# Kernel tuning notes

Measured on AMD Instinct MI355X. Metric: run time of the kernel, lower is better.

Reference implementation:

```python
import jax, jax.numpy as jnp
import numpy as np

N, C, V, L = 32, 32, 400, 64
GH_IN, GH = 64, [128, 64]
NUM_GRAPHS, ORDER, K, ALPHA = 2, 2, 20, 0.05
OUT_CH = 32
CAT_CH = C * (NUM_GRAPHS * ORDER + 1)
BN_EPS = 1e-5


def setup_inputs() -> dict:
    key = jax.random.key(0)
    ks = jax.random.split(key, 12)
    s = lambda fan_in: 1.0 / np.sqrt(fan_in)
    return {
        "inputs": jax.random.normal(ks[0], (N, C, V, L), jnp.float32),
        "adj_mats": jax.random.normal(ks[1], (V, V, GH_IN), jnp.float32),
        # edge MLP: Linear(64->128), ReLU, Linear(128->64), ReLU, Linear(64->num_graphs)
        "mlp_w0": jax.random.normal(ks[2], (GH_IN, GH[0]), jnp.float32) * s(GH_IN),
        "mlp_b0": jnp.zeros((GH[0],), jnp.float32),
        "mlp_w1": jax.random.normal(ks[3], (GH[0], GH[1]), jnp.float32) * s(GH[0]),
        "mlp_b1": jnp.zeros((GH[1],), jnp.float32),
        "mlp_w2": jax.random.normal(ks[4], (GH[1], NUM_GRAPHS), jnp.float32) * s(GH[1]),
        "mlp_b2": jnp.zeros((NUM_GRAPHS,), jnp.float32),
        # 1x1 Conv2d(in=160, out=32) == channel-mixing matmul
        "conv_w": jax.random.normal(ks[5], (OUT_CH, CAT_CH), jnp.float32) * s(CAT_CH),
        "conv_b": jnp.zeros((OUT_CH,), jnp.float32),
        "bn_gamma": jnp.ones((OUT_CH,), jnp.float32),
        "bn_beta": jnp.zeros((OUT_CH,), jnp.float32),
    }


def _sparsify(logits):
    # logits: [V, V]; softmax over rows, keep top-K per row, renormalize.
    adj = jax.nn.softmax(logits, axis=1)
    _, idx = jax.lax.top_k(adj, K)                     # [V, K]
    mask = jnp.zeros((V, V), adj.dtype).at[jnp.arange(V)[:, None], idx].set(1.0)
    adj = adj * mask
    return adj / (adj.sum(axis=1, keepdims=True) + 1e-8)


def reference(inputs, adj_mats, mlp_w0, mlp_b0, mlp_w1, mlp_b1, mlp_w2, mlp_b2,
              conv_w, conv_b, bn_gamma, bn_beta):
    # edge MLP on [V, V, GH_IN] -> [V, V, NUM_GRAPHS]
    h = jax.nn.relu(adj_mats @ mlp_w0 + mlp_b0)
    h = jax.nn.relu(h @ mlp_w1 + mlp_b1)
    g = h @ mlp_w2 + mlp_b2
    A = jax.vmap(_sparsify)(jnp.moveaxis(g, 2, 0))     # [NUM_GRAPHS, V, V]

    x = jax.nn.relu(inputs)                            # [N, C, V, L]
    outs = [x]
    for i in range(NUM_GRAPHS):
        y = x
        for _ in range(ORDER):
            y = ALPHA * x + (1.0 - ALPHA) * jnp.einsum('ncvl,vw->ncwl', y, A[i])
            outs.append(y)
    x1 = jnp.concatenate(outs, axis=1)                 # [N, CAT_CH, V, L]
    out = jnp.einsum('ncvl,oc->novl', x1, conv_w) + conv_b[None, :, None, None]

    # BatchNorm2d, training mode (batch statistics, biased variance)
    mean = out.mean(axis=(0, 2, 3), keepdims=True)
    var = out.var(axis=(0, 2, 3), keepdims=True)
    out = (out - mean) * jax.lax.rsqrt(var + BN_EPS)
    out = out * bn_gamma[None, :, None, None] + bn_beta[None, :, None, None]
    return out
```

## Files before the change

kernel.cpp:

```cpp
#include <hip/hip_runtime.h>


#define VDIM 400
#define VP   416
#define KV   (4*VP)
#define EROWS (5*VP)
#define OL   2048
#define ALPHA_ 0.05f
#define BETA_  0.95f

typedef short  bf16x8 __attribute__((ext_vector_type(8)));
typedef float  f32x4  __attribute__((ext_vector_type(4)));

__device__ inline unsigned short f2bf(float x){
  unsigned int u = __float_as_uint(x);
  unsigned int r = (u + 0x7fffu + ((u >> 16) & 1u)) >> 16;
  return (unsigned short)r;
}
__device__ inline float bf2f(unsigned short u){
  return __uint_as_float(((unsigned int)u) << 16);
}

__global__ __launch_bounds__(256) void k_mlp3(
    const float* __restrict__ adj,
    const float* __restrict__ w0, const float* __restrict__ b0,
    const float* __restrict__ w1, const float* __restrict__ b1,
    const float* __restrict__ w2, const float* __restrict__ b2,
    float* __restrict__ g)
{
  __shared__ __align__(16) float s_inT[64*68];
  __shared__ __align__(16) float s_h1 [64*72];
  __shared__ __align__(16) float s_red[4*64*2];
  const int tid  = threadIdx.x;
  const long ebase = (long)blockIdx.x * 64;
  const int wid  = __builtin_amdgcn_readfirstlane(tid >> 6);
  const int lane = tid & 63;

  #pragma unroll
  for (int i = 0; i < 4; ++i){
    const int idx = tid + i*256;
    const int row = idx >> 4, f4 = (idx & 15)*4;
    f32x4 v = *reinterpret_cast<const f32x4*>(&adj[(ebase + row)*64 + f4]);
    s_inT[(f4+0)*68 + row] = v.x;
    s_inT[(f4+1)*68 + row] = v.y;
    s_inT[(f4+2)*68 + row] = v.z;
    s_inT[(f4+3)*68 + row] = v.w;
  }
  __syncthreads();

  const int n0 = wid * 32;
  float h0[32];
  #pragma unroll
  for (int j = 0; j < 32; ++j) h0[j] = b0[n0 + j];
  #pragma unroll 2
  for (int f = 0; f < 64; ++f){
    const float a = s_inT[f*68 + lane];
    const float* __restrict__ wr = &w0[f*128 + n0];
    #pragma unroll
    for (int j = 0; j < 32; ++j) h0[j] = fmaf(a, wr[j], h0[j]);
  }
  #pragma unroll
  for (int j = 0; j < 32; ++j) h0[j] = fmaxf(h0[j], 0.f);

  float p[64];
  #pragma unroll
  for (int nh = 0; nh < 2; ++nh){
    float acc1[32];
    #pragma unroll
    for (int j = 0; j < 32; ++j) acc1[j] = 0.f;
    #pragma unroll 2
    for (int f = 0; f < 32; ++f){
      const float hv = h0[f];
      const float* __restrict__ wr = &w1[(n0 + f)*64 + nh*32];
      #pragma unroll
      for (int j = 0; j < 32; ++j) acc1[j] = fmaf(hv, wr[j], acc1[j]);
    }
    #pragma unroll
    for (int j = 0; j < 32; ++j) p[nh*32 + j] = acc1[j];
  }

  #pragma unroll
  for (int w = 0; w < 4; ++w){
    if (wid == w){
      if (w == 0){
        #pragma unroll
        for (int j = 0; j < 64; j += 4){
          f32x4 v = { p[j] + b1[j],   p[j+1] + b1[j+1],
                      p[j+2] + b1[j+2], p[j+3] + b1[j+3] };
          *reinterpret_cast<f32x4*>(&s_h1[lane*72 + j]) = v;
        }
      } else {
        #pragma unroll
        for (int j = 0; j < 64; j += 4){
          f32x4 v = *reinterpret_cast<f32x4*>(&s_h1[lane*72 + j]);
          v.x += p[j]; v.y += p[j+1]; v.z += p[j+2]; v.w += p[j+3];
          *reinterpret_cast<f32x4*>(&s_h1[lane*72 + j]) = v;
        }
      }
    }
    __syncthreads();
  }

  float q0 = 0.f, q1 = 0.f;
  #pragma unroll
  for (int j = 0; j < 16; ++j){
    const int n = wid*16 + j;
    const float hv = fmaxf(s_h1[lane*72 + n], 0.f);
    q0 = fmaf(hv, w2[n*2 + 0], q0);
    q1 = fmaf(hv, w2[n*2 + 1], q1);
  }
  s_red[(wid*64 + lane)*2 + 0] = q0;
  s_red[(wid*64 + lane)*2 + 1] = q1;
  __syncthreads();
  if (wid == 0){
    float r0 = b2[0], r1 = b2[1];
    #pragma unroll
    for (int w = 0; w < 4; ++w){
      r0 += s_red[(w*64 + lane)*2 + 0];
      r1 += s_red[(w*64 + lane)*2 + 1];
    }
    g[(ebase + lane)*2 + 0] = r0;
    g[(ebase + lane)*2 + 1] = r1;
  }
}

__global__ __launch_bounds__(256) void k_sparsify(
    const float* __restrict__ g, float* __restrict__ Bf)
{
  const int row = blockIdx.x, gr = blockIdx.y, tid = threadIdx.x;
  const int wid = tid >> 6, lane = tid & 63;
  __shared__ float s_v[4]; __shared__ int s_i[4];
  __shared__ float s_p[512];
  __shared__ int   s_sel[512];
  const int i0 = tid, i1 = tid + 256;
  float v0 = (i0 < VDIM) ? g[(row*VDIM + i0)*2 + gr] : -3.4e38f;
  float v1 = (i1 < VDIM) ? g[(row*VDIM + i1)*2 + gr] : -3.4e38f;

  float m = fmaxf(v0, v1);
  for (int off = 32; off > 0; off >>= 1) m = fmaxf(m, __shfl_down(m, off, 64));
  if (lane == 0) s_v[wid] = m;
  __syncthreads();
  const float rowmax = fmaxf(fmaxf(s_v[0], s_v[1]), fmaxf(s_v[2], s_v[3]));
  float p0 = (i0 < VDIM) ? expf(v0 - rowmax) : 0.f;
  float p1 = (i1 < VDIM) ? expf(v1 - rowmax) : 0.f;
  float zs = p0 + p1;
  for (int off = 32; off > 0; off >>= 1) zs += __shfl_down(zs, off, 64);
  __syncthreads();
  if (lane == 0) s_v[wid] = zs;
  __syncthreads();
  const float Z = s_v[0] + s_v[1] + s_v[2] + s_v[3];
  p0 /= Z; p1 /= Z;
  s_p[i0] = p0; s_p[i1] = p1;
  s_sel[i0] = (i0 < VDIM) ? 0 : 1;
  s_sel[i1] = (i1 < VDIM) ? 0 : 1;
  __syncthreads();

  float ssum = 0.f;
  for (int it = 0; it < 20; ++it){
    float cv = -1.f; int ci = 0x7fffffff;
    if (!s_sel[i0])              { cv = p0; ci = i0; }
    if (!s_sel[i1] && (p1 > cv)) { cv = p1; ci = i1; }
    for (int off = 32; off > 0; off >>= 1){
      float ov = __shfl_down(cv, off, 64); int oi = __shfl_down(ci, off, 64);
      if (ov > cv || (ov == cv && oi < ci)){ cv = ov; ci = oi; }
    }
    if (lane == 0){ s_v[wid] = cv; s_i[wid] = ci; }
    __syncthreads();
    float wv = s_v[0]; int wi_ = s_i[0];
    #pragma unroll
    for (int k = 1; k < 4; ++k){
      float ov = s_v[k]; int oi = s_i[k];
      if (ov > wv || (ov == wv && oi < wi_)){ wv = ov; wi_ = oi; }
    }
    ssum += wv;
    if (tid == (wi_ & 255)) s_sel[wi_] = 1;
    __syncthreads();
  }
  const float inv = 1.0f / (ssum + 1e-8f);
  float* B1 = Bf + (size_t)(gr*2) * (VDIM*VDIM);
  if (i0 < VDIM) B1[(size_t)i0*VDIM + row] = s_sel[i0] ? (s_p[i0]*inv) : 0.f;
  if (i1 < VDIM) B1[(size_t)i1*VDIM + row] = s_sel[i1] ? (s_p[i1]*inv) : 0.f;
}

__global__ __launch_bounds__(256) void k_sq(float* __restrict__ Bf)
{
  const int gr = blockIdx.z;
  const float* S = Bf + (size_t)(2*gr)   * (VDIM*VDIM);
  float*       D = Bf + (size_t)(2*gr+1) * (VDIM*VDIM);
  const int tx = threadIdx.x & 15, ty = threadIdx.x >> 4;
  const int w = blockIdx.x*16 + ty, v = blockIdx.y*16 + tx;
  __shared__ float As[16][17], Bs[16][17];
  float acc = 0.f;
  for (int u0 = 0; u0 < VDIM; u0 += 16){
    As[ty][tx] = S[(size_t)w*VDIM + u0 + tx];
    Bs[ty][tx] = S[(size_t)(u0+ty)*VDIM + v];
    __syncthreads();
    #pragma unroll
    for (int u = 0; u < 16; ++u) acc += As[ty][u] * Bs[u][tx];
    __syncthreads();
  }
  D[(size_t)w*VDIM + v] = acc;
}

__global__ __launch_bounds__(256) void k_pack(
    const float* __restrict__ Bf, const float* __restrict__ conv_w,
    unsigned short* __restrict__ Bcat, unsigned short* __restrict__ Mpp,
    float* __restrict__ bns)
{
  const int idx = blockIdx.x*256 + threadIdx.x;
  if (idx < 512*KV){
    const int w = idx / KV, col = idx % KV;
    const int k1 = col / VP, v = col % VP;
    float val = (w < VDIM && v < VDIM) ? Bf[(size_t)k1*(VDIM*VDIM) + (size_t)w*VDIM + v] : 0.f;
    Bcat[idx] = f2bf(val);
  }
  if (blockIdx.x == 0){
    const float a = ALPHA_, b = BETA_;
    for (int mIdx = threadIdx.x; mIdx < 160*32; mIdx += 256){
      const int rowm = mIdx >> 5, c = mIdx & 31;
      const int k = rowm / 32, o = rowm & 31;
      float W[5];
      #pragma unroll
      for (int j = 0; j < 5; ++j) W[j] = conv_w[o*160 + j*32 + c];
      float val;
      if      (k == 0) val = W[0] + a*(W[1]+W[2]+W[3]+W[4]);
      else if (k == 1) val = b*W[1] + a*b*W[2];
      else if (k == 2) val = b*b*W[2];
      else if (k == 3) val = b*W[3] + a*b*W[4];
      else             val = b*b*W[4];
      Mpp[rowm*32 + c] = f2bf(val);
    }
    if (threadIdx.x < 64) bns[threadIdx.x] = 0.f;
  }
}

__global__ __launch_bounds__(640) void k_e(
    const float* __restrict__ x, const unsigned short* __restrict__ Mpp,
    unsigned short* __restrict__ e, int n0)
{
  const int v = blockIdx.x;
  const int n = n0 + blockIdx.y;
  const int tid = threadIdx.x;
  unsigned short* en = e + (size_t)blockIdx.y * EROWS * OL;
  if (v >= VDIM){
    for (int i = tid; i < 5*256; i += 640){
      const int k = i >> 8, off = (i & 255) * 8;
      *reinterpret_cast<uint4*>(&en[(size_t)(k*VP + v)*OL + off]) = make_uint4(0,0,0,0);
    }
    return;
  }
  __shared__ __align__(16) unsigned short s_xT[64*32];
  __shared__ __align__(16) unsigned short s_out[10*16*64];
  if (tid < 512){
    const int c = tid >> 4, l4 = (tid & 15) * 4;
    float4 xv = *reinterpret_cast<const float4*>(x + ((size_t)n*32 + c)*25600 + (size_t)v*64 + l4);
    s_xT[(l4+0)*32 + c] = f2bf(fmaxf(xv.x, 0.f));
    s_xT[(l4+1)*32 + c] = f2bf(fmaxf(xv.y, 0.f));
    s_xT[(l4+2)*32 + c] = f2bf(fmaxf(xv.z, 0.f));
    s_xT[(l4+3)*32 + c] = f2bf(fmaxf(xv.w, 0.f));
  }
  __syncthreads();
  const int wid = tid >> 6, lane = tid & 63;
  const int l15 = lane & 15, q = lane >> 4;
  const int m0 = wid * 16;
  bf16x8 afrag = *reinterpret_cast<const bf16x8*>(&Mpp[(m0 + l15)*32 + q*8]);
  const f32x4 zero = {0.f, 0.f, 0.f, 0.f};
  f32x4 acc[4];
  #pragma unroll
  for (int lt = 0; lt < 4; ++lt){
    bf16x8 bfrag = *reinterpret_cast<const bf16x8*>(&s_xT[(lt*16 + l15)*32 + q*8]);
    acc[lt] = __builtin_amdgcn_mfma_f32_16x16x32_bf16(afrag, bfrag, zero, 0, 0, 0);
  }
  unsigned short* so = &s_out[wid*1024];
  #pragma unroll
  for (int lt = 0; lt < 4; ++lt)
    #pragma unroll
    for (int r = 0; r < 4; ++r)
      so[(q*4 + r)*64 + lt*16 + l15] = f2bf(acc[lt][r]);
  const int k = wid >> 1, o0 = (wid & 1) * 16;
  const size_t gbase = (size_t)(k*VP + v)*OL + (size_t)o0*64;
  uint4 d0 = *reinterpret_cast<uint4*>(&so[lane*16]);
  uint4 d1 = *reinterpret_cast<uint4*>(&so[lane*16 + 8]);
  *reinterpret_cast<uint4*>(&en[gbase + lane*16])     = d0;
  *reinterpret_cast<uint4*>(&en[gbase + lane*16 + 8]) = d1;
}

__global__ __launch_bounds__(256) void k_prop(
    const unsigned short* __restrict__ Bcat, const unsigned short* __restrict__ e,
    const float* __restrict__ conv_b, float* __restrict__ out,
    float* __restrict__ bns, int n0)
{
  const int mt = blockIdx.x, nt = blockIdx.y, np = blockIdx.z;
  const int tid = threadIdx.x;
  const int wid = tid >> 6, lane = tid & 63;
  const int l15 = lane & 15, q = lane >> 4;
  const int ww = wid & 1, wh = wid >> 1;
  const unsigned short* en = e + (size_t)np * EROWS * OL;
  __shared__ __align__(16) unsigned short s_a[128*40];
  __shared__ __align__(16) unsigned short s_b[128*32];
  const f32x4 zero = {0.f, 0.f, 0.f, 0.f};
  f32x4 acc[4][4];
  #pragma unroll
  for (int mi = 0; mi < 4; ++mi)
    #pragma unroll
    for (int ni = 0; ni < 4; ++ni) acc[mi][ni] = zero;
  const int w_base = mt*128, ol0 = nt*128;

  for (int kk = 0; kk < KV; kk += 32){
    #pragma unroll
    for (int i = 0; i < 2; ++i){
      const int idx = tid + i*256;
      const int m = idx >> 2, seg = idx & 3;
      uint4 d = *reinterpret_cast<const uint4*>(&Bcat[(size_t)(w_base + m)*KV + kk + seg*8]);
      *reinterpret_cast<uint4*>(&s_a[m*40 + seg*8]) = d;
    }
    #pragma unroll
    for (int i = 0; i < 2; ++i){
      const int idx = tid + i*256;
      const int r = idx >> 4, seg = idx & 15;
      union { uint4 u; unsigned short s[8]; } d;
      d.u = *reinterpret_cast<const uint4*>(&en[(size_t)(VP + kk + r)*OL + ol0 + seg*8]);
      const int kb = r >> 3, kin = r & 7;
      #pragma unroll
      for (int t = 0; t < 8; ++t){
        const int nn = seg*8 + t;
        s_b[nn*32 + ((kb ^ ((nn >> 3) & 3)) << 3) + kin] = d.s[t];
      }
    }
    __syncthreads();
    bf16x8 af[4], bfr[4];
    #pragma unroll
    for (int mi = 0; mi < 4; ++mi){
      const int m = ww*64 + mi*16 + l15;
      af[mi] = *reinterpret_cast<const bf16x8*>(&s_a[m*40 + q*8]);
    }
    #pragma unroll
    for (int ni = 0; ni < 4; ++ni){
      const int nn = wh*64 + ni*16 + l15;
      bfr[ni] = *reinterpret_cast<const bf16x8*>(&s_b[nn*32 + ((q ^ ((nn >> 3) & 3)) << 3)]);
    }
    #pragma unroll
    for (int mi = 0; mi < 4; ++mi)
      #pragma unroll
      for (int ni = 0; ni < 4; ++ni)
        acc[mi][ni] = __builtin_amdgcn_mfma_f32_16x16x32_bf16(af[mi], bfr[ni], acc[mi][ni], 0, 0, 0);
    __syncthreads();
  }

  const int n_g = n0 + np;
  const int o = (ol0 >> 6) + wh;
  const float cb = conv_b[o];
  float bsum = 0.f, bsq = 0.f;
  #pragma unroll
  for (int mi = 0; mi < 4; ++mi){
    #pragma unroll
    for (int ni = 0; ni < 4; ++ni){
      const int nloc = wh*64 + ni*16 + l15;
      const int ol = ol0 + nloc;
      const int l = ol & 63;
      #pragma unroll
      for (int r = 0; r < 4; ++r){
        const int w = w_base + ww*64 + mi*16 + q*4 + r;
        if (w < VDIM){
          float val = acc[mi][ni][r] + bf2f(en[(size_t)w*OL + ol]) + cb;
          out[(((size_t)n_g*32 + o)*VDIM + w)*64 + l] = val;
          bsum += val; bsq += val*val;
        }
      }
    }
  }
  for (int off = 32; off > 0; off >>= 1){
    bsum += __shfl_down(bsum, off, 64);
    bsq  += __shfl_down(bsq,  off, 64);
  }
  if (lane == 0){
    atomicAdd(&bns[o], bsum);
    atomicAdd(&bns[32 + o], bsq);
  }
}

__global__ __launch_bounds__(256) void k_bnapply(
    float* __restrict__ out, const float* __restrict__ bns,
    const float* __restrict__ gamma, const float* __restrict__ beta, int total4)
{
  const int idx = blockIdx.x*256 + threadIdx.x;
  if (idx >= total4) return;
  const int o = (int)(((long)idx*4 / 25600) & 31);
  const float invM = 1.f / 819200.f;
  const float mean = bns[o] * invM;
  const float var  = bns[32+o] * invM - mean*mean;
  const float inv  = 1.0f / sqrtf(var + 1e-5f);
  const float sc = inv * gamma[o];
  const float sh = beta[o] - mean * sc;
  float4 v = reinterpret_cast<float4*>(out)[idx];
  v.x = v.x*sc + sh; v.y = v.y*sc + sh; v.z = v.z*sc + sh; v.w = v.w*sc + sh;
  reinterpret_cast<float4*>(out)[idx] = v;
}

extern "C" void kernel_launch(void* const* d_in, const int* in_sizes, int n_in,
                              void* d_out, int out_size, void* d_ws, size_t ws_size,
                              hipStream_t stream)
{
  const float* x      = (const float*)d_in[0];
  const float* adj    = (const float*)d_in[1];
  const float* w0     = (const float*)d_in[2];
  const float* b0     = (const float*)d_in[3];
  const float* w1     = (const float*)d_in[4];
  const float* b1     = (const float*)d_in[5];
  const float* w2     = (const float*)d_in[6];
  const float* b2     = (const float*)d_in[7];
  const float* conv_w = (const float*)d_in[8];
  const float* conv_b = (const float*)d_in[9];
  const float* gamma  = (const float*)d_in[10];
  const float* beta   = (const float*)d_in[11];
  float* out = (float*)d_out;

  char* ws = (char*)d_ws;
  size_t off = 0;
  auto alloc = [&](size_t bytes) -> void* {
    void* p = ws + off;
    off = (off + bytes + 255) & ~(size_t)255;
    return p;
  };
  float*          g_   = (float*)         alloc((size_t)VDIM*VDIM*2*4);
  float*          Bf   = (float*)         alloc((size_t)4*VDIM*VDIM*4);
  unsigned short* Bcat = (unsigned short*)alloc((size_t)512*KV*2);
  unsigned short* Mpp  = (unsigned short*)alloc((size_t)160*32*2);
  float*          bns  = (float*)         alloc((size_t)64*4);
  const size_t per_n = (size_t)EROWS * OL * 2;
  size_t avail = (ws_size > off) ? (ws_size - off) : 0;
  int NC = (int)(avail / per_n);
  if (NC > 8) NC = 8;
  if (NC < 1) NC = 1;
  while (32 % NC) NC--;
  unsigned short* ebuf = (unsigned short*)(ws + off);

  k_mlp3<<<2500, 256, 0, stream>>>(adj, w0, b0, w1, b1, w2, b2, g_);
  k_sparsify<<<dim3(VDIM, 2), 256, 0, stream>>>(g_, Bf);
  k_sq<<<dim3(25, 25, 2), 256, 0, stream>>>(Bf);
  k_pack<<<(512*KV + 255)/256, 256, 0, stream>>>(Bf, conv_w, Bcat, Mpp, bns);
  for (int n0 = 0; n0 < 32; n0 += NC){
    k_e<<<dim3(VP, NC), 640, 0, stream>>>(x, Mpp, ebuf, n0);
    k_prop<<<dim3(4, 16, NC), 256, 0, stream>>>(Bcat, ebuf, conv_b, out, bns, n0);
  }
  k_bnapply<<<(26214400/4 + 255)/256, 256, 0, stream>>>(out, bns, gamma, beta, 26214400/4);
}
```

Measured before the change: 778.3 us.

## Double-buffer LDS tiles in k_prop and transpose B via packed register stores

```diff
diff --git a/kernel.cpp b/kernel.cpp
--- a/kernel.cpp
+++ b/kernel.cpp
@@ -296,8 +296,8 @@
   const int l15 = lane & 15, q = lane >> 4;
   const int ww = wid & 1, wh = wid >> 1;
   const unsigned short* en = e + (size_t)np * EROWS * OL;
-  __shared__ __align__(16) unsigned short s_a[128*40];
-  __shared__ __align__(16) unsigned short s_b[128*32];
+  __shared__ __align__(16) unsigned short s_a[2][128*40];
+  __shared__ __align__(16) unsigned short s_b[2][128*40];
   const f32x4 zero = {0.f, 0.f, 0.f, 0.f};
   f32x4 acc[4][4];
   #pragma unroll
@@ -306,45 +306,73 @@
     for (int ni = 0; ni < 4; ++ni) acc[mi][ni] = zero;
   const int w_base = mt*128, ol0 = nt*128;
 
-  for (int kk = 0; kk < KV; kk += 32){
+  const int brg = tid >> 6;
+  const int bnb = tid & 63;
+
+  uint4        aR[2];
+  unsigned int bR[8];
+
+  auto LOADG = [&](int kk){
     #pragma unroll
     for (int i = 0; i < 2; ++i){
       const int idx = tid + i*256;
       const int m = idx >> 2, seg = idx & 3;
-      uint4 d = *reinterpret_cast<const uint4*>(&Bcat[(size_t)(w_base + m)*KV + kk + seg*8]);
-      *reinterpret_cast<uint4*>(&s_a[m*40 + seg*8]) = d;
-    }
+      aR[i] = *reinterpret_cast<const uint4*>(&Bcat[(size_t)(w_base + m)*KV + kk + seg*8]);
+    }
+    #pragma unroll
+    for (int i = 0; i < 8; ++i)
+      bR[i] = *reinterpret_cast<const unsigned int*>(
+                 &en[(size_t)(VP + kk + brg*8 + i)*OL + ol0 + bnb*2]);
+  };
+  auto STORES = [&](int buf){
     #pragma unroll
     for (int i = 0; i < 2; ++i){
       const int idx = tid + i*256;
-      const int r = idx >> 4, seg = idx & 15;
-      union { uint4 u; unsigned short s[8]; } d;
-      d.u = *reinterpret_cast<const uint4*>(&en[(size_t)(VP + kk + r)*OL + ol0 + seg*8]);
-      const int kb = r >> 3, kin = r & 7;
-      #pragma unroll
-      for (int t = 0; t < 8; ++t){
-        const int nn = seg*8 + t;
-        s_b[nn*32 + ((kb ^ ((nn >> 3) & 3)) << 3) + kin] = d.s[t];
-      }
-    }
-    __syncthreads();
+      const int m = idx >> 2, seg = idx & 3;
+      *reinterpret_cast<uint4*>(&s_a[buf][m*40 + seg*8]) = aR[i];
+    }
+    uint4 t;
+    t.x = (bR[0] & 0xffffu) | (bR[1] << 16);
+    t.y = (bR[2] & 0xffffu) | (bR[3] << 16);
+    t.z = (bR[4] & 0xffffu) | (bR[5] << 16);
+    t.w = (bR[6] & 0xffffu) | (bR[7] << 16);
+    *reinterpret_cast<uint4*>(&s_b[buf][(bnb*2 + 0)*40 + brg*8]) = t;
+    t.x = (bR[0] >> 16) | (bR[1] & 0xffff0000u);
+    t.y = (bR[2] >> 16) | (bR[3] & 0xffff0000u);
+    t.z = (bR[4] >> 16) | (bR[5] & 0xffff0000u);
+    t.w = (bR[6] >> 16) | (bR[7] & 0xffff0000u);
+    *reinterpret_cast<uint4*>(&s_b[buf][(bnb*2 + 1)*40 + brg*8]) = t;
+  };
+
+  LOADG(0);
+  STORES(0);
+  __syncthreads();
+  int cur = 0;
+
+  for (int kk = 0; kk < KV; kk += 32){
+    const bool more = (kk + 32 < KV);
+    if (more) LOADG(kk + 32);
+
     bf16x8 af[4], bfr[4];
     #pragma unroll
     for (int mi = 0; mi < 4; ++mi){
       const int m = ww*64 + mi*16 + l15;
-      af[mi] = *reinterpret_cast<const bf16x8*>(&s_a[m*40 + q*8]);
+      af[mi] = *reinterpret_cast<const bf16x8*>(&s_a[cur][m*40 + q*8]);
     }
     #pragma unroll
     for (int ni = 0; ni < 4; ++ni){
       const int nn = wh*64 + ni*16 + l15;
-      bfr[ni] = *reinterpret_cast<const bf16x8*>(&s_b[nn*32 + ((q ^ ((nn >> 3) & 3)) << 3)]);
+      bfr[ni] = *reinterpret_cast<const bf16x8*>(&s_b[cur][nn*40 + q*8]);
     }
     #pragma unroll
     for (int mi = 0; mi < 4; ++mi)
       #pragma unroll
       for (int ni = 0; ni < 4; ++ni)
         acc[mi][ni] = __builtin_amdgcn_mfma_f32_16x16x32_bf16(af[mi], bfr[ni], acc[mi][ni], 0, 0, 0);
-    __syncthreads();
+
+    if (more) STORES(cur ^ 1);
+    __syncthreads();
+    cur ^= 1;
   }
 
   const int n_g = n0 + np;
```

Result: slower. 810.0 us (+4.1%).
